# Optimization experiments

Measured on AMD Instinct MI355X. Metric: run time of the kernel, lower is better.

## Reference

```python
import jax, jax.numpy as jnp
import numpy as np

N_NODES = 50000
DEG = 16
N_EDGES = N_NODES * DEG
H = 8
D = 32
NEG_SLOPE = 0.2


def setup_inputs() -> dict:
    key = jax.random.key(0)
    k1, k2, k3, k4 = jax.random.split(key, 4)
    feat = jax.random.normal(k1, (N_NODES, H * D), dtype=jnp.float32)
    attn_l = jax.random.normal(k2, (1, H, D), dtype=jnp.float32) * 0.1
    attn_r = jax.random.normal(k3, (1, H, D), dtype=jnp.float32) * 0.1
    bias = jnp.zeros((H * D,), dtype=jnp.float32)
    # every dst node has in-degree DEG (no zero-in-degree nodes)
    dst = jnp.repeat(jnp.arange(N_NODES, dtype=jnp.int32), DEG)
    src = jax.random.randint(k4, (N_EDGES,), 0, N_NODES, dtype=jnp.int32)
    return {"feat": feat, "attn_l": attn_l, "attn_r": attn_r, "bias": bias,
            "src": src, "dst": dst}


def reference(feat, attn_l, attn_r, bias, src, dst):
    N = feat.shape[0]
    fs = feat.reshape(N, H, D)                      # [N,H,D]
    el = (fs * attn_l).sum(-1)                      # [N,H]
    er = (fs * attn_r).sum(-1)                      # [N,H]
    # per-edge attention logit: u_add_v + leaky_relu
    e = jax.nn.leaky_relu(el[src] + er[dst], negative_slope=NEG_SLOPE)  # [E,H]
    # segmented (per-dst) softmax over incoming edges
    emax = jax.ops.segment_max(e, dst, num_segments=N)  # [N,H]
    ee = jnp.exp(e - emax[dst])                         # [E,H]
    esum = jax.ops.segment_sum(ee, dst, num_segments=N)  # [N,H]
    a = ee / esum[dst]                                  # [E,H]
    # u_mul_e then sum: weighted scatter-aggregate
    msg = fs[src] * a[:, :, None]                       # [E,H,D]
    rst = jax.ops.segment_sum(msg, dst, num_segments=N)  # [N,H,D]
    rst = rst + bias.reshape(1, H, D)
    return rst
```

## Files before the change

### kernel.cpp

```cpp
#include <hip/hip_runtime.h>
#include <hip/hip_fp16.h>

#define HEADS 8
#define DIM 32
#define DEGREE 16
#define NEG_SLOPE 0.2f

template <bool WRITE_F16>
__global__ __launch_bounds__(256) void elr_kernel(
    const float4* __restrict__ feat4,
    const float4* __restrict__ attn_l4,
    const float4* __restrict__ attn_r4,
    float* __restrict__ el8, float* __restrict__ er8,
    ushort4* __restrict__ featbH, int total4, int N) {
  int t = blockIdx.x * 256 + threadIdx.x;
  if (t >= total4) return;
  float4 v = feat4[t];
  int c4 = t & 63;
  float4 al = attn_l4[c4];
  float4 ar = attn_r4[c4];
  float pl = v.x * al.x + v.y * al.y + v.z * al.z + v.w * al.w;
  float pr = v.x * ar.x + v.y * ar.y + v.z * ar.z + v.w * ar.w;
#pragma unroll
  for (int off = 4; off >= 1; off >>= 1) {
    pl += __shfl_xor(pl, off);
    pr += __shfl_xor(pr, off);
  }
  if ((t & 7) == 0) {
    el8[t >> 3] = pl;
    er8[t >> 3] = pr;
  }
  if (WRITE_F16) {
    ushort4 b;
    b.x = __half_as_ushort(__float2half_rn(v.x));
    b.y = __half_as_ushort(__float2half_rn(v.y));
    b.z = __half_as_ushort(__float2half_rn(v.z));
    b.w = __half_as_ushort(__float2half_rn(v.w));
    int n = t >> 6, h = c4 >> 3, d4 = c4 & 7;
    featbH[((size_t)h * N + n) * 8 + d4] = b;
  }
}

__global__ __launch_bounds__(256) void weights_kernel(
    const float4* __restrict__ el84,
    const float4* __restrict__ er84,
    const int* __restrict__ srcIdx,
    __half* __restrict__ wHh, int N) {
  int t = threadIdx.x;
  int n0 = blockIdx.x * 16;
  int nl = t >> 4;
  int n = n0 + nl;
  if (n >= N) return;
  int s = srcIdx[n0 * DEGREE + t];
  float4 e0 = el84[(size_t)s * 2], e1 = el84[(size_t)s * 2 + 1];
  float4 r0 = er84[(size_t)n * 2], r1 = er84[(size_t)n * 2 + 1];
  float l[HEADS] = {e0.x + r0.x, e0.y + r0.y, e0.z + r0.z, e0.w + r0.w,
                    e1.x + r1.x, e1.y + r1.y, e1.z + r1.z, e1.w + r1.w};
  float w[HEADS];
#pragma unroll
  for (int h = 0; h < HEADS; h++) {
    float e = l[h];
    e = e > 0.0f ? e : NEG_SLOPE * e;
    float m = e;
#pragma unroll
    for (int off = 8; off >= 1; off >>= 1) m = fmaxf(m, __shfl_xor(m, off));
    float x = __expf(e - m);
    float ssum = x;
#pragma unroll
    for (int off = 8; off >= 1; off >>= 1) ssum += __shfl_xor(ssum, off);
    w[h] = x / ssum;
  }
#pragma unroll
  for (int h = 0; h < HEADS; h++)
    wHh[(size_t)h * N * DEGREE + n0 * DEGREE + t] = __float2half_rn(w[h]);
}

__global__ __launch_bounds__(256) void gat_kernel(
    const uint4* __restrict__ featbH4,
    const uint4* __restrict__ wHh4,
    const int4* __restrict__ src4,
    const float* __restrict__ bias,
    float* __restrict__ out, int N) {
  int h = blockIdx.x & 7;
  int chunk = blockIdx.x >> 3;
  int t = threadIdx.x;
  int nl = t >> 2, c = t & 3;
  int n = chunk * 64 + nl;
  if (n >= N) return;

  int4 s0 = src4[(size_t)n * 4 + 0];
  int4 s1 = src4[(size_t)n * 4 + 1];
  int4 s2 = src4[(size_t)n * 4 + 2];
  int4 s3 = src4[(size_t)n * 4 + 3];
  uint4 w0 = wHh4[((size_t)h * N + n) * 2 + 0];
  uint4 w1 = wHh4[((size_t)h * N + n) * 2 + 1];

  const __half2 z = __float2half2_rn(0.0f);
  __half2 a0 = z, a1 = z, a2 = z, a3 = z;
  __half2 b0 = z, b1 = z, b2 = z, b3 = z;

  size_t hbase = (size_t)h * N;

#define GAT_EDGE(sv, wu, hi, A0, A1, A2, A3)                                 \
  do {                                                                       \
    uint4 r = featbH4[(hbase + (unsigned)(sv)) * 4 + c];                     \
    unsigned short wb = (unsigned short)((hi) ? ((wu) >> 16) : ((wu) & 0xffffu)); \
    __half2 wj = __half2half2(__ushort_as_half(wb));                         \
    A0 = __hfma2(wj, *(const __half2*)&r.x, A0);                             \
    A1 = __hfma2(wj, *(const __half2*)&r.y, A1);                             \
    A2 = __hfma2(wj, *(const __half2*)&r.z, A2);                             \
    A3 = __hfma2(wj, *(const __half2*)&r.w, A3);                             \
  } while (0)

#pragma unroll
  for (int dummy = 0; dummy < 1; dummy++) {
    GAT_EDGE(s0.x, w0.x, 0, a0, a1, a2, a3);
    GAT_EDGE(s0.y, w0.x, 1, a0, a1, a2, a3);
    GAT_EDGE(s0.z, w0.y, 0, a0, a1, a2, a3);
    GAT_EDGE(s0.w, w0.y, 1, a0, a1, a2, a3);
    GAT_EDGE(s1.x, w0.z, 0, a0, a1, a2, a3);
    GAT_EDGE(s1.y, w0.z, 1, a0, a1, a2, a3);
    GAT_EDGE(s1.z, w0.w, 0, a0, a1, a2, a3);
    GAT_EDGE(s1.w, w0.w, 1, a0, a1, a2, a3);
    GAT_EDGE(s2.x, w1.x, 0, b0, b1, b2, b3);
    GAT_EDGE(s2.y, w1.x, 1, b0, b1, b2, b3);
    GAT_EDGE(s2.z, w1.y, 0, b0, b1, b2, b3);
    GAT_EDGE(s2.w, w1.y, 1, b0, b1, b2, b3);
    GAT_EDGE(s3.x, w1.z, 0, b0, b1, b2, b3);
    GAT_EDGE(s3.y, w1.z, 1, b0, b1, b2, b3);
    GAT_EDGE(s3.z, w1.w, 0, b0, b1, b2, b3);
    GAT_EDGE(s3.w, w1.w, 1, b0, b1, b2, b3);
  }
#undef GAT_EDGE

  float2 f0 = __half22float2(a0), g0 = __half22float2(b0);
  float2 f1 = __half22float2(a1), g1 = __half22float2(b1);
  float2 f2 = __half22float2(a2), g2 = __half22float2(b2);
  float2 f3 = __half22float2(a3), g3 = __half22float2(b3);

  const float4* bias4 = (const float4*)bias;
  int bidx = h * 8 + c * 2;
  float4 bb0 = bias4[bidx], bb1 = bias4[bidx + 1];
  float4 o0 = make_float4(f0.x + g0.x + bb0.x, f0.y + g0.y + bb0.y,
                          f1.x + g1.x + bb0.z, f1.y + g1.y + bb0.w);
  float4 o1 = make_float4(f2.x + g2.x + bb1.x, f2.y + g2.y + bb1.y,
                          f3.x + g3.x + bb1.z, f3.y + g3.y + bb1.w);
  size_t o = (size_t)n * 64 + h * 8 + c * 2;
  ((float4*)out)[o] = o0;
  ((float4*)out)[o + 1] = o1;
}

__global__ __launch_bounds__(256) void gat_fused_kernel(
    const uint4* __restrict__ featbH4,
    const float* __restrict__ el8,
    const float* __restrict__ er8,
    const int* __restrict__ srcIdx,
    const float* __restrict__ bias,
    float* __restrict__ out, int N) {
  int h = blockIdx.x & 7;
  int chunk = blockIdx.x >> 3;
  int t = threadIdx.x;
  int n0 = chunk * 16;
  int n = n0 + (t >> 4);
  if (n >= N) return;
  int sidx = srcIdx[n0 * DEGREE + t];
  float e = el8[(size_t)sidx * 8 + h] + er8[(size_t)n * 8 + h];
  e = e > 0.0f ? e : NEG_SLOPE * e;
  float m = e;
#pragma unroll
  for (int off = 8; off >= 1; off >>= 1) m = fmaxf(m, __shfl_xor(m, off));
  float x = __expf(e - m);
  float ssum = x;
#pragma unroll
  for (int off = 8; off >= 1; off >>= 1) ssum += __shfl_xor(ssum, off);
  float w = x / ssum;

  int lane = t & 63;
  int q = (lane >> 2) & 3;
  int c = lane & 3;
  int base = lane & 48;
  float acc[8];
#pragma unroll
  for (int k = 0; k < 8; k++) acc[k] = 0.0f;
#pragma unroll
  for (int p = 0; p < 4; p++) {
    int j = p * 4 + q;
    int sj = __shfl(sidx, base + j);
    float wj = __shfl(w, base + j);
    uint4 r = featbH4[((size_t)h * N + sj) * 4 + c];
    float2 v0 = __half22float2(*(const __half2*)&r.x);
    float2 v1 = __half22float2(*(const __half2*)&r.y);
    float2 v2 = __half22float2(*(const __half2*)&r.z);
    float2 v3 = __half22float2(*(const __half2*)&r.w);
    acc[0] += wj * v0.x;
    acc[1] += wj * v0.y;
    acc[2] += wj * v1.x;
    acc[3] += wj * v1.y;
    acc[4] += wj * v2.x;
    acc[5] += wj * v2.y;
    acc[6] += wj * v3.x;
    acc[7] += wj * v3.y;
  }
#pragma unroll
  for (int k = 0; k < 8; k++) {
    acc[k] += __shfl_xor(acc[k], 4);
    acc[k] += __shfl_xor(acc[k], 8);
  }
  if (q == 0) {
    const float4* bias4 = (const float4*)bias;
    int bidx = h * 8 + c * 2;
    float4 b0 = bias4[bidx], b1 = bias4[bidx + 1];
    float4 o0 = make_float4(acc[0] + b0.x, acc[1] + b0.y,
                            acc[2] + b0.z, acc[3] + b0.w);
    float4 o1 = make_float4(acc[4] + b1.x, acc[5] + b1.y,
                            acc[6] + b1.z, acc[7] + b1.w);
    size_t o = (size_t)n * 64 + h * 8 + c * 2;
    ((float4*)out)[o] = o0;
    ((float4*)out)[o + 1] = o1;
  }
}

extern "C" void kernel_launch(void* const* d_in, const int* in_sizes, int n_in,
                              void* d_out, int out_size, void* d_ws, size_t ws_size,
                              hipStream_t stream) {
  const float* feat   = (const float*)d_in[0];
  const float* attn_l = (const float*)d_in[1];
  const float* attn_r = (const float*)d_in[2];
  const float* bias   = (const float*)d_in[3];
  const int*   src    = (const int*)d_in[4];
  float* out = (float*)d_out;

  int total = in_sizes[0];
  int N = total / (HEADS * DIM);
  int total4 = total / 4;
  int nchunks16 = (N + 15) / 16;
  int nchunks64 = (N + 63) / 64;

  float* el8 = (float*)d_ws;
  float* er8 = el8 + (size_t)N * HEADS;
  ushort4* featbH = (ushort4*)(er8 + (size_t)N * HEADS);
  __half* wHh = (__half*)((char*)featbH + (size_t)total * 2);

  size_t need_base = (size_t)N * HEADS * 2 * sizeof(float);
  size_t need_feat = need_base + (size_t)total * 2;
  size_t need_full = need_feat + (size_t)N * DEGREE * HEADS * sizeof(__half);

  if (ws_size >= need_full) {
    elr_kernel<true><<<(total4 + 255) / 256, 256, 0, stream>>>(
        (const float4*)feat, (const float4*)attn_l, (const float4*)attn_r,
        el8, er8, featbH, total4, N);
    weights_kernel<<<nchunks16, 256, 0, stream>>>(
        (const float4*)el8, (const float4*)er8, src, wHh, N);
    gat_kernel<<<nchunks64 * 8, 256, 0, stream>>>(
        (const uint4*)featbH, (const uint4*)wHh, (const int4*)src, bias, out, N);
  } else {
    elr_kernel<true><<<(total4 + 255) / 256, 256, 0, stream>>>(
        (const float4*)feat, (const float4*)attn_l, (const float4*)attn_r,
        el8, er8, featbH, total4, N);
    gat_fused_kernel<<<nchunks16 * 8, 256, 0, stream>>>(
        (const uint4*)featbH, el8, er8, src, bias, out, N);
  }
}
```

Before: 161.7 us.

## Interleave fp16 features by head pairs to widen gather rows

Changes the fp16 feature copy from a per-head layout to one where two adjacent heads are stored contiguously per node, giving 128-byte rows. The aggregation kernel now has 8 threads per node cover two heads, so each edge gather reads one wider contiguous segment instead of two separate 64-byte ones. This aims to raise memory-transaction efficiency for the random source gathers. In exchange each block covers fewer nodes, and the weight loads are now per-thread for two heads.

```diff
diff --git a/kernel.cpp b/kernel.cpp
--- a/kernel.cpp
+++ b/kernel.cpp
@@ -6,13 +6,12 @@
 #define DEGREE 16
 #define NEG_SLOPE 0.2f
 
-template <bool WRITE_F16>
 __global__ __launch_bounds__(256) void elr_kernel(
     const float4* __restrict__ feat4,
     const float4* __restrict__ attn_l4,
     const float4* __restrict__ attn_r4,
     float* __restrict__ el8, float* __restrict__ er8,
-    ushort4* __restrict__ featbH, int total4, int N) {
+    ushort4* __restrict__ featb2, int total4, int N) {
   int t = blockIdx.x * 256 + threadIdx.x;
   if (t >= total4) return;
   float4 v = feat4[t];
@@ -30,15 +29,13 @@
     el8[t >> 3] = pl;
     er8[t >> 3] = pr;
   }
-  if (WRITE_F16) {
-    ushort4 b;
-    b.x = __half_as_ushort(__float2half_rn(v.x));
-    b.y = __half_as_ushort(__float2half_rn(v.y));
-    b.z = __half_as_ushort(__float2half_rn(v.z));
-    b.w = __half_as_ushort(__float2half_rn(v.w));
-    int n = t >> 6, h = c4 >> 3, d4 = c4 & 7;
-    featbH[((size_t)h * N + n) * 8 + d4] = b;
-  }
+  ushort4 b;
+  b.x = __half_as_ushort(__float2half_rn(v.x));
+  b.y = __half_as_ushort(__float2half_rn(v.y));
+  b.z = __half_as_ushort(__float2half_rn(v.z));
+  b.w = __half_as_ushort(__float2half_rn(v.w));
+  int n = t >> 6, h = c4 >> 3, d4 = c4 & 7;
+  featb2[(((size_t)(h >> 1) * N + n) * 16) + (h & 1) * 8 + d4] = b;
 }
 
 __global__ __launch_bounds__(256) void weights_kernel(
@@ -76,17 +73,20 @@
 }
 
 __global__ __launch_bounds__(256) void gat_kernel(
-    const uint4* __restrict__ featbH4,
+    const uint4* __restrict__ featb2q,
     const uint4* __restrict__ wHh4,
     const int4* __restrict__ src4,
     const float* __restrict__ bias,
     float* __restrict__ out, int N) {
-  int h = blockIdx.x & 7;
-  int chunk = blockIdx.x >> 3;
+  int p = blockIdx.x & 3;
+  int chunk = blockIdx.x >> 2;
   int t = threadIdx.x;
-  int nl = t >> 2, c = t & 3;
-  int n = chunk * 64 + nl;
+  int nl = t >> 3, c8 = t & 7;
+  int n = chunk * 32 + nl;
   if (n >= N) return;
+
+  int h = p * 2 + (c8 >> 2);
+  int dq = c8 & 3;
 
   int4 s0 = src4[(size_t)n * 4 + 0];
   int4 s1 = src4[(size_t)n * 4 + 1];
@@ -99,11 +99,11 @@
   __half2 a0 = z, a1 = z, a2 = z, a3 = z;
   __half2 b0 = z, b1 = z, b2 = z, b3 = z;
 
-  size_t hbase = (size_t)h * N;
+  size_t pbase = (size_t)p * N;
 
 #define GAT_EDGE(sv, wu, hi, A0, A1, A2, A3)                                 \
   do {                                                                       \
-    uint4 r = featbH4[(hbase + (unsigned)(sv)) * 4 + c];                     \
+    uint4 r = featb2q[(pbase + (unsigned)(sv)) * 8 + c8];                    \
     unsigned short wb = (unsigned short)((hi) ? ((wu) >> 16) : ((wu) & 0xffffu)); \
     __half2 wj = __half2half2(__ushort_as_half(wb));                         \
     A0 = __hfma2(wj, *(const __half2*)&r.x, A0);                             \
@@ -112,25 +112,22 @@
     A3 = __hfma2(wj, *(const __half2*)&r.w, A3);                             \
   } while (0)
 
-#pragma unroll
-  for (int dummy = 0; dummy < 1; dummy++) {
-    GAT_EDGE(s0.x, w0.x, 0, a0, a1, a2, a3);
-    GAT_EDGE(s0.y, w0.x, 1, a0, a1, a2, a3);
-    GAT_EDGE(s0.z, w0.y, 0, a0, a1, a2, a3);
-    GAT_EDGE(s0.w, w0.y, 1, a0, a1, a2, a3);
-    GAT_EDGE(s1.x, w0.z, 0, a0, a1, a2, a3);
-    GAT_EDGE(s1.y, w0.z, 1, a0, a1, a2, a3);
-    GAT_EDGE(s1.z, w0.w, 0, a0, a1, a2, a3);
-    GAT_EDGE(s1.w, w0.w, 1, a0, a1, a2, a3);
-    GAT_EDGE(s2.x, w1.x, 0, b0, b1, b2, b3);
-    GAT_EDGE(s2.y, w1.x, 1, b0, b1, b2, b3);
-    GAT_EDGE(s2.z, w1.y, 0, b0, b1, b2, b3);
-    GAT_EDGE(s2.w, w1.y, 1, b0, b1, b2, b3);
-    GAT_EDGE(s3.x, w1.z, 0, b0, b1, b2, b3);
-    GAT_EDGE(s3.y, w1.z, 1, b0, b1, b2, b3);
-    GAT_EDGE(s3.z, w1.w, 0, b0, b1, b2, b3);
-    GAT_EDGE(s3.w, w1.w, 1, b0, b1, b2, b3);
-  }
+  GAT_EDGE(s0.x, w0.x, 0, a0, a1, a2, a3);
+  GAT_EDGE(s0.y, w0.x, 1, a0, a1, a2, a3);
+  GAT_EDGE(s0.z, w0.y, 0, a0, a1, a2, a3);
+  GAT_EDGE(s0.w, w0.y, 1, a0, a1, a2, a3);
+  GAT_EDGE(s1.x, w0.z, 0, a0, a1, a2, a3);
+  GAT_EDGE(s1.y, w0.z, 1, a0, a1, a2, a3);
+  GAT_EDGE(s1.z, w0.w, 0, a0, a1, a2, a3);
+  GAT_EDGE(s1.w, w0.w, 1, a0, a1, a2, a3);
+  GAT_EDGE(s2.x, w1.x, 0, b0, b1, b2, b3);
+  GAT_EDGE(s2.y, w1.x, 1, b0, b1, b2, b3);
+  GAT_EDGE(s2.z, w1.y, 0, b0, b1, b2, b3);
+  GAT_EDGE(s2.w, w1.y, 1, b0, b1, b2, b3);
+  GAT_EDGE(s3.x, w1.z, 0, b0, b1, b2, b3);
+  GAT_EDGE(s3.y, w1.z, 1, b0, b1, b2, b3);
+  GAT_EDGE(s3.z, w1.w, 0, b0, b1, b2, b3);
+  GAT_EDGE(s3.w, w1.w, 1, b0, b1, b2, b3);
 #undef GAT_EDGE
 
   float2 f0 = __half22float2(a0), g0 = __half22float2(b0);
@@ -139,19 +136,19 @@
   float2 f3 = __half22float2(a3), g3 = __half22float2(b3);
 
   const float4* bias4 = (const float4*)bias;
-  int bidx = h * 8 + c * 2;
+  int bidx = h * 8 + dq * 2;
   float4 bb0 = bias4[bidx], bb1 = bias4[bidx + 1];
   float4 o0 = make_float4(f0.x + g0.x + bb0.x, f0.y + g0.y + bb0.y,
                           f1.x + g1.x + bb0.z, f1.y + g1.y + bb0.w);
   float4 o1 = make_float4(f2.x + g2.x + bb1.x, f2.y + g2.y + bb1.y,
                           f3.x + g3.x + bb1.z, f3.y + g3.y + bb1.w);
-  size_t o = (size_t)n * 64 + h * 8 + c * 2;
+  size_t o = (size_t)n * 64 + h * 8 + dq * 2;
   ((float4*)out)[o] = o0;
   ((float4*)out)[o + 1] = o1;
 }
 
 __global__ __launch_bounds__(256) void gat_fused_kernel(
-    const uint4* __restrict__ featbH4,
+    const uint4* __restrict__ featb2q,
     const float* __restrict__ el8,
     const float* __restrict__ er8,
     const int* __restrict__ srcIdx,
@@ -183,11 +180,11 @@
 #pragma unroll
   for (int k = 0; k < 8; k++) acc[k] = 0.0f;
 #pragma unroll
-  for (int p = 0; p < 4; p++) {
-    int j = p * 4 + q;
+  for (int pp = 0; pp < 4; pp++) {
+    int j = pp * 4 + q;
     int sj = __shfl(sidx, base + j);
     float wj = __shfl(w, base + j);
-    uint4 r = featbH4[((size_t)h * N + sj) * 4 + c];
+    uint4 r = featb2q[(((size_t)(h >> 1) * N + sj) * 8) + (h & 1) * 4 + c];
     float2 v0 = __half22float2(*(const __half2*)&r.x);
     float2 v1 = __half22float2(*(const __half2*)&r.y);
     float2 v2 = __half22float2(*(const __half2*)&r.z);
@@ -234,30 +231,30 @@
   int N = total / (HEADS * DIM);
   int total4 = total / 4;
   int nchunks16 = (N + 15) / 16;
-  int nchunks64 = (N + 63) / 64;
+  int nchunks32 = (N + 31) / 32;
 
   float* el8 = (float*)d_ws;
   float* er8 = el8 + (size_t)N * HEADS;
-  ushort4* featbH = (ushort4*)(er8 + (size_t)N * HEADS);
-  __half* wHh = (__half*)((char*)featbH + (size_t)total * 2);
+  ushort4* featb2 = (ushort4*)(er8 + (size_t)N * HEADS);
+  __half* wHh = (__half*)((char*)featb2 + (size_t)total * 2);
 
   size_t need_base = (size_t)N * HEADS * 2 * sizeof(float);
   size_t need_feat = need_base + (size_t)total * 2;
   size_t need_full = need_feat + (size_t)N * DEGREE * HEADS * sizeof(__half);
 
   if (ws_size >= need_full) {
-    elr_kernel<true><<<(total4 + 255) / 256, 256, 0, stream>>>(
+    elr_kernel<<<(total4 + 255) / 256, 256, 0, stream>>>(
         (const float4*)feat, (const float4*)attn_l, (const float4*)attn_r,
-        el8, er8, featbH, total4, N);
+        el8, er8, featb2, total4, N);
     weights_kernel<<<nchunks16, 256, 0, stream>>>(
         (const float4*)el8, (const float4*)er8, src, wHh, N);
-    gat_kernel<<<nchunks64 * 8, 256, 0, stream>>>(
-        (const uint4*)featbH, (const uint4*)wHh, (const int4*)src, bias, out, N);
+    gat_kernel<<<nchunks32 * 4, 256, 0, stream>>>(
+        (const uint4*)featb2, (const uint4*)wHh, (const int4*)src, bias, out, N);
   } else {
-    elr_kernel<true><<<(total4 + 255) / 256, 256, 0, stream>>>(
+    elr_kernel<<<(total4 + 255) / 256, 256, 0, stream>>>(
         (const float4*)feat, (const float4*)attn_l, (const float4*)attn_r,
-        el8, er8, featbH, total4, N);
+        el8, er8, featb2, total4, N);
     gat_fused_kernel<<<nchunks16 * 8, 256, 0, stream>>>(
-        (const uint4*)featbH, el8, er8, src, bias, out, N);
-  }
-}
+        (const uint4*)featb2, el8, er8, src, bias, out, N);
+  }
+}
```

Measured after the change: 159.4 us. Within noise of the previous version (-1.4%).
